# Optimization experiments

Hardware: AMD Instinct MI355X
Metric: run time of the kernel (lower is better)

Reference implementation:

```python
import jax, jax.numpy as jnp
import numpy as np
import math

BS, N, DX, H = 4, 256, 256, 8
DF = DX // H
DFF = 1024
EPS = 1e-5


def layer_norm(x, g, b):
    mu = jnp.mean(x, axis=-1, keepdims=True)
    var = jnp.var(x, axis=-1, keepdims=True)
    return (x - mu) * jax.lax.rsqrt(var + EPS) * g + b


def setup_inputs() -> dict:
    key = jax.random.key(0)
    ks = jax.random.split(key, 16)
    s = 1.0 / math.sqrt(DX)
    inp = {
        "X": jax.random.normal(ks[0], (BS, N, DX), jnp.float32),
        "e_add": jax.random.normal(ks[1], (BS, N, N, DX), jnp.float32),
        "e_mul": jax.random.normal(ks[2], (BS, N, N, DX), jnp.float32),
        "y_x_add": jax.random.normal(ks[3], (BS, DX), jnp.float32),
        "y_x_mul": jax.random.normal(ks[4], (BS, DX), jnp.float32),
        "node_mask": jnp.ones((BS, N), jnp.float32),
        "Wq": jax.random.normal(ks[5], (DX, DX), jnp.float32) * s,
        "bq": jnp.zeros((DX,), jnp.float32),
        "Wk": jax.random.normal(ks[6], (DX, DX), jnp.float32) * s,
        "bk": jnp.zeros((DX,), jnp.float32),
        "Wv": jax.random.normal(ks[7], (DX, DX), jnp.float32) * s,
        "bv": jnp.zeros((DX,), jnp.float32),
        "Wo": jax.random.normal(ks[8], (DX, DX), jnp.float32) * s,
        "bo": jnp.zeros((DX,), jnp.float32),
        "W1": jax.random.normal(ks[9], (DX, DFF), jnp.float32) * s,
        "b1": jnp.zeros((DFF,), jnp.float32),
        "W2": jax.random.normal(ks[10], (DFF, DX), jnp.float32) * (1.0 / math.sqrt(DFF)),
        "b2": jnp.zeros((DX,), jnp.float32),
        "g1": jnp.ones((DX,), jnp.float32),
        "beta1": jnp.zeros((DX,), jnp.float32),
        "g2": jnp.ones((DX,), jnp.float32),
        "beta2": jnp.zeros((DX,), jnp.float32),
    }
    return inp


def reference(X, e_add, e_mul, y_x_add, y_x_mul, node_mask,
              Wq, bq, Wk, bk, Wv, bv, Wo, bo, W1, b1, W2, b2,
              g1, beta1, g2, beta2):
    bs, n, dx = X.shape
    x_mask = node_mask[:, :, None]                      # (bs,n,1)
    e_mask1 = x_mask[:, :, None, :]                     # (bs,n,1,1)
    e_mask2 = x_mask[:, None, :, :]                     # (bs,1,n,1)

    Q = ((X @ Wq + bq) * x_mask).reshape(bs, n, H, DF)
    K = ((X @ Wk + bk) * x_mask).reshape(bs, n, H, DF)
    V = ((X @ Wv + bv) * x_mask).reshape(bs, n, H, DF)

    # elementwise QK: (bs,n,n,H,df)
    Y = Q[:, :, None] * K[:, None, :] / math.sqrt(DF)

    ee = (e_mask1 * e_mask2)[..., None]                 # (bs,n,n,1,1)
    E1 = (e_mul[..., None, :].reshape(bs, n, n, H, DF) if False else e_mul.reshape(bs, n, n, H, DF)) * ee
    E2 = e_add.reshape(bs, n, n, H, DF) * ee
    Y = Y * (E1 + 1.0) + E2

    # masked softmax over key axis (axis=2); mask from e_mask2 per head
    smask = node_mask[:, None, :, None, None] > 0       # (bs,1,n,1,1)
    Y = jnp.where(smask, Y, -jnp.inf)
    attn = jax.nn.softmax(Y, axis=2)

    weighted_V = jnp.sum(attn * V[:, None], axis=2).reshape(bs, n, dx)

    newX = y_x_add[:, None, :] + (y_x_mul[:, None, :] + 1.0) * weighted_V
    newX = ((newX @ Wo + bo)) * x_mask

    X1 = layer_norm(X + newX, g1, beta1)
    ffo = jax.nn.relu(X1 @ W1 + b1) @ W2 + b2
    X2 = layer_norm(X1 + ffo, g2, beta2)
    return X2
```

## Files before the change

### kernel.cpp

```cpp
#include <hip/hip_runtime.h>
#include <hip/hip_bf16.h>
#include <cstdint>

#define BSZ 4
#define NN 256
#define DXC 256
#define DFFC 1024
#define ROWS (BSZ*NN)

template <int EPI>
__global__ __launch_bounds__(256) void gemm32(
    const float* __restrict__ A,
    const float* __restrict__ B0, const float* __restrict__ B1,
    const float* __restrict__ B2,
    const float* __restrict__ bias0, const float* __restrict__ bias1,
    const float* __restrict__ bias2,
    float* __restrict__ C0, float* __restrict__ C1, float* __restrict__ C2,
    const float* __restrict__ mask,
    int M, int Nn, int K)
{
    const float* B = B0; const float* bias = bias0; float* C = C0;
    if (blockIdx.z == 1) { B = B1; bias = bias1; C = C1; }
    if (blockIdx.z == 2) { B = B2; bias = bias2; C = C2; }

    __shared__ float As[32][36];
    __shared__ float Bs[32][36];

    const int tid  = threadIdx.x;
    const int row0 = blockIdx.y * 32;
    const int col0 = blockIdx.x * 32;
    const int tx = tid & 15, ty = tid >> 4;

    const int la_r = tid >> 3;
    const int la_k = (tid & 7) * 4;

    float acc00 = 0.f, acc01 = 0.f, acc10 = 0.f, acc11 = 0.f;

    for (int k0 = 0; k0 < K; k0 += 32) {
        *(float4*)&As[la_r][la_k] = *(const float4*)(A + (size_t)(row0 + la_r) * K + (k0 + la_k));
        *(float4*)&Bs[la_r][la_k] = *(const float4*)(B + (size_t)(k0 + la_r) * Nn + (col0 + la_k));
        __syncthreads();
        #pragma unroll
        for (int k = 0; k < 32; ++k) {
            float a0v = As[2*ty][k],   a1v = As[2*ty+1][k];
            float b0v = Bs[k][2*tx],   b1v = Bs[k][2*tx+1];
            acc00 += a0v * b0v; acc01 += a0v * b1v;
            acc10 += a1v * b0v; acc11 += a1v * b1v;
        }
        __syncthreads();
    }

    const int r0 = row0 + 2*ty, c0 = col0 + 2*tx;
    const float bi0 = bias[c0], bi1 = bias[c0 + 1];
    float v00 = acc00 + bi0, v01 = acc01 + bi1;
    float v10 = acc10 + bi0, v11 = acc11 + bi1;
    if constexpr (EPI == 1) {
        float m0 = mask[r0], m1 = mask[r0 + 1];
        v00 *= m0; v01 *= m0; v10 *= m1; v11 *= m1;
    } else if constexpr (EPI == 2) {
        v00 = fmaxf(v00, 0.f); v01 = fmaxf(v01, 0.f);
        v10 = fmaxf(v10, 0.f); v11 = fmaxf(v11, 0.f);
    }
    C[(size_t)r0 * Nn + c0]       = v00; C[(size_t)r0 * Nn + c0 + 1]       = v01;
    C[(size_t)(r0+1) * Nn + c0]   = v10; C[(size_t)(r0+1) * Nn + c0 + 1]   = v11;
}

__global__ __launch_bounds__(256) void attn_kernel(
    const float* __restrict__ Qb, const float* __restrict__ Kb, const float* __restrict__ Vb,
    const float* __restrict__ e_add, const float* __restrict__ e_mul,
    const float* __restrict__ y_x_add, const float* __restrict__ y_x_mul,
    const float* __restrict__ nmask,
    float* __restrict__ nXi)
{
    const int row  = blockIdx.x;
    const int b    = row >> 8;
    const int tid  = threadIdx.x;
    const int wv   = tid >> 6;
    const int lane = tid & 63;
    const int hd   = lane << 2;

    const float mi = nmask[row];
    float4 q = *(const float4*)(Qb + (size_t)row * DXC + hd);
    const float inv = 0.17677669529663687f;
    q.x *= inv; q.y *= inv; q.z *= inv; q.w *= inv;

    const float* ea_p = e_add + (size_t)row * NN * DXC + hd;
    const float* em_p = e_mul + (size_t)row * NN * DXC + hd;
    const float* kp = Kb + (size_t)(b << 8) * DXC + hd;
    const float* vp = Vb + (size_t)(b << 8) * DXC + hd;
    const float* mp = nmask + (b << 8);

    float l0=0.f,l1=0.f,l2=0.f,l3=0.f;
    float a0=0.f,a1=0.f,a2=0.f,a3=0.f;

    #pragma unroll 4
    for (int j = wv; j < NN; j += 4) {
        const float mj = mp[j];
        const float ee = mi * mj;
        const float4 k4 = *(const float4*)(kp + (size_t)j * DXC);
        const float4 v4 = *(const float4*)(vp + (size_t)j * DXC);
        const float4 em = *(const float4*)(em_p + (size_t)j * DXC);
        const float4 ea = *(const float4*)(ea_p + (size_t)j * DXC);
        float y0 = (q.x*k4.x) * (em.x*ee + 1.f) + ea.x*ee;
        float y1 = (q.y*k4.y) * (em.y*ee + 1.f) + ea.y*ee;
        float y2 = (q.z*k4.z) * (em.z*ee + 1.f) + ea.z*ee;
        float y3 = (q.w*k4.w) * (em.w*ee + 1.f) + ea.w*ee;
        if (!(mj > 0.f)) { y0 = y1 = y2 = y3 = -1e30f; }
        const float p0 = __expf(y0), p1 = __expf(y1), p2 = __expf(y2), p3 = __expf(y3);
        l0 += p0; l1 += p1; l2 += p2; l3 += p3;
        a0 += p0*v4.x; a1 += p1*v4.y; a2 += p2*v4.z; a3 += p3*v4.w;
    }

    __shared__ float sl[4][256];
    __shared__ float sa[4][256];
    *(float4*)&sl[wv][hd] = make_float4(l0, l1, l2, l3);
    *(float4*)&sa[wv][hd] = make_float4(a0, a1, a2, a3);
    __syncthreads();

    const int c = tid;
    const float L = sl[0][c] + sl[1][c] + sl[2][c] + sl[3][c];
    const float A = sa[0][c] + sa[1][c] + sa[2][c] + sa[3][c];
    const float wV = A / L;
    const float yxa = y_x_add[b * DXC + c];
    const float yxm = y_x_mul[b * DXC + c];
    nXi[(size_t)row * DXC + c] = yxa + (yxm + 1.f) * wV;
}

__global__ __launch_bounds__(256) void ln_kernel(
    const float* __restrict__ base, const float* __restrict__ delta,
    const float* __restrict__ g, const float* __restrict__ be,
    float* __restrict__ out)
{
    const int row = blockIdx.x, t = threadIdx.x;
    const size_t idx = (size_t)row * DXC + t;
    const float s = base[idx] + delta[idx];
    __shared__ float red[8];
    float sum = s, sq = s * s;
    #pragma unroll
    for (int o = 32; o > 0; o >>= 1) { sum += __shfl_down(sum, o); sq += __shfl_down(sq, o); }
    if ((t & 63) == 0) { red[t >> 6] = sum; red[4 + (t >> 6)] = sq; }
    __syncthreads();
    sum = red[0] + red[1] + red[2] + red[3];
    sq  = red[4] + red[5] + red[6] + red[7];
    const float mean = sum * (1.f / DXC);
    const float var  = sq * (1.f / DXC) - mean * mean;
    const float r = rsqrtf(var + 1e-5f);
    out[idx] = (s - mean) * r * g[t] + be[t];
}

extern "C" void kernel_launch(void* const* d_in, const int* in_sizes, int n_in,
                              void* d_out, int out_size, void* d_ws, size_t ws_size,
                              hipStream_t stream)
{
    const float* X       = (const float*)d_in[0];
    const float* e_add   = (const float*)d_in[1];
    const float* e_mul   = (const float*)d_in[2];
    const float* y_x_add = (const float*)d_in[3];
    const float* y_x_mul = (const float*)d_in[4];
    const float* nmask   = (const float*)d_in[5];
    const float* Wq = (const float*)d_in[6];
    const float* bq = (const float*)d_in[7];
    const float* Wk = (const float*)d_in[8];
    const float* bk = (const float*)d_in[9];
    const float* Wv = (const float*)d_in[10];
    const float* bv = (const float*)d_in[11];
    const float* Wo = (const float*)d_in[12];
    const float* bo = (const float*)d_in[13];
    const float* W1 = (const float*)d_in[14];
    const float* b1 = (const float*)d_in[15];
    const float* W2 = (const float*)d_in[16];
    const float* b2 = (const float*)d_in[17];
    const float* g1 = (const float*)d_in[18];
    const float* be1= (const float*)d_in[19];
    const float* g2 = (const float*)d_in[20];
    const float* be2= (const float*)d_in[21];

    float* ws  = (float*)d_ws;
    float* Qb  = ws + 0 * 262144;
    float* Kb  = ws + 1 * 262144;
    float* Vb  = ws + 2 * 262144;
    float* nXi = ws + 3 * 262144;
    float* nXo = ws + 4 * 262144;
    float* X1b = ws + 5 * 262144;
    float* ffo = ws + 6 * 262144;
    float* hb  = ws + 7 * 262144;

    gemm32<1><<<dim3(DXC/32, ROWS/32, 3), 256, 0, stream>>>(
        X, Wq, Wk, Wv, bq, bk, bv, Qb, Kb, Vb, nmask, ROWS, DXC, DXC);

    attn_kernel<<<dim3(ROWS), 256, 0, stream>>>(
        Qb, Kb, Vb, e_add, e_mul, y_x_add, y_x_mul, nmask, nXi);

    gemm32<1><<<dim3(DXC/32, ROWS/32, 1), 256, 0, stream>>>(
        nXi, Wo, Wo, Wo, bo, bo, bo, nXo, nXo, nXo, nmask, ROWS, DXC, DXC);

    ln_kernel<<<dim3(ROWS), 256, 0, stream>>>(X, nXo, g1, be1, X1b);

    gemm32<2><<<dim3(DFFC/32, ROWS/32, 1), 256, 0, stream>>>(
        X1b, W1, W1, W1, b1, b1, b1, hb, hb, hb, nullptr, ROWS, DFFC, DXC);

    gemm32<0><<<dim3(DXC/32, ROWS/32, 1), 256, 0, stream>>>(
        hb, W2, W2, W2, b2, b2, b2, ffo, ffo, ffo, nullptr, ROWS, DXC, DFFC);

    ln_kernel<<<dim3(ROWS), 256, 0, stream>>>(X1b, ffo, g2, be2, (float*)d_out);
}
```

Baseline: 626.8 us.

## Use 64x64 register-blocked double-buffered GEMM and widen attention to 512 threads

Replaces the 32x32 GEMM with 64x64 tiles in which each thread computes a 4x4 register block. The A tile is stored transposed in shared memory, and the global loads for the next k-tile are prefetched into registers while the current tile is computed. The attention kernel moves to 512 threads (8 waves), and each iteration handles two key rows so more e_add/e_mul loads are in flight, aiming to get closer to memory bandwidth on the large edge tensors. The trade-off is fewer GEMM blocks, which may underfill the GPU on the small matrices, plus more registers per thread in both kernels.

```diff
diff --git a/kernel.cpp b/kernel.cpp
--- a/kernel.cpp
+++ b/kernel.cpp
@@ -1,5 +1,4 @@
 #include <hip/hip_runtime.h>
-#include <hip/hip_bf16.h>
 #include <cstdint>
 
 #define BSZ 4
@@ -9,7 +8,7 @@
 #define ROWS (BSZ*NN)
 
 template <int EPI>
-__global__ __launch_bounds__(256) void gemm32(
+__global__ __launch_bounds__(256) void gemm64(
     const float* __restrict__ A,
     const float* __restrict__ B0, const float* __restrict__ B1,
     const float* __restrict__ B2,
@@ -23,49 +22,102 @@
     if (blockIdx.z == 1) { B = B1; bias = bias1; C = C1; }
     if (blockIdx.z == 2) { B = B2; bias = bias2; C = C2; }
 
-    __shared__ float As[32][36];
-    __shared__ float Bs[32][36];
+    __shared__ float As[2][32][68];
+    __shared__ float Bs[2][32][68];
 
     const int tid  = threadIdx.x;
-    const int row0 = blockIdx.y * 32;
-    const int col0 = blockIdx.x * 32;
-    const int tx = tid & 15, ty = tid >> 4;
-
-    const int la_r = tid >> 3;
-    const int la_k = (tid & 7) * 4;
-
-    float acc00 = 0.f, acc01 = 0.f, acc10 = 0.f, acc11 = 0.f;
-
-    for (int k0 = 0; k0 < K; k0 += 32) {
-        *(float4*)&As[la_r][la_k] = *(const float4*)(A + (size_t)(row0 + la_r) * K + (k0 + la_k));
-        *(float4*)&Bs[la_r][la_k] = *(const float4*)(B + (size_t)(k0 + la_r) * Nn + (col0 + la_k));
-        __syncthreads();
+    const int row0 = blockIdx.y * 64;
+    const int col0 = blockIdx.x * 64;
+    const int tx4 = (tid & 15) * 4;
+    const int ty4 = (tid >> 4) * 4;
+
+    const int ar = tid >> 3;
+    const int ak = (tid & 7) * 4;
+    const int br = tid >> 4;
+    const int bn = (tid & 15) * 4;
+
+    const float* Ap  = A + (size_t)(row0 + ar) * K + ak;
+    const float* Ap2 = A + (size_t)(row0 + 32 + ar) * K + ak;
+    const float* Bp  = B + (size_t)br * Nn + col0 + bn;
+    const float* Bp2 = B + (size_t)(br + 16) * Nn + col0 + bn;
+
+    float4 a0 = *(const float4*)Ap;
+    float4 a1 = *(const float4*)Ap2;
+    float4 b0 = *(const float4*)Bp;
+    float4 b1 = *(const float4*)Bp2;
+
+    float acc[4][4] = {};
+
+    As[0][ak+0][ar] = a0.x; As[0][ak+1][ar] = a0.y;
+    As[0][ak+2][ar] = a0.z; As[0][ak+3][ar] = a0.w;
+    As[0][ak+0][ar+32] = a1.x; As[0][ak+1][ar+32] = a1.y;
+    As[0][ak+2][ar+32] = a1.z; As[0][ak+3][ar+32] = a1.w;
+    *(float4*)&Bs[0][br][bn]      = b0;
+    *(float4*)&Bs[0][br+16][bn]   = b1;
+    __syncthreads();
+
+    const int nt = K >> 5;
+    for (int t = 0; t < nt; ++t) {
+        const int cur = t & 1, nxt = cur ^ 1;
+        const bool more = (t + 1 < nt);
+        if (more) {
+            const int k0 = (t + 1) << 5;
+            a0 = *(const float4*)(Ap + k0);
+            a1 = *(const float4*)(Ap2 + k0);
+            b0 = *(const float4*)(Bp + (size_t)k0 * Nn);
+            b1 = *(const float4*)(Bp2 + (size_t)k0 * Nn);
+        }
         #pragma unroll
         for (int k = 0; k < 32; ++k) {
-            float a0v = As[2*ty][k],   a1v = As[2*ty+1][k];
-            float b0v = Bs[k][2*tx],   b1v = Bs[k][2*tx+1];
-            acc00 += a0v * b0v; acc01 += a0v * b1v;
-            acc10 += a1v * b0v; acc11 += a1v * b1v;
-        }
-        __syncthreads();
-    }
-
-    const int r0 = row0 + 2*ty, c0 = col0 + 2*tx;
-    const float bi0 = bias[c0], bi1 = bias[c0 + 1];
-    float v00 = acc00 + bi0, v01 = acc01 + bi1;
-    float v10 = acc10 + bi0, v11 = acc11 + bi1;
-    if constexpr (EPI == 1) {
-        float m0 = mask[r0], m1 = mask[r0 + 1];
-        v00 *= m0; v01 *= m0; v10 *= m1; v11 *= m1;
-    } else if constexpr (EPI == 2) {
-        v00 = fmaxf(v00, 0.f); v01 = fmaxf(v01, 0.f);
-        v10 = fmaxf(v10, 0.f); v11 = fmaxf(v11, 0.f);
-    }
-    C[(size_t)r0 * Nn + c0]       = v00; C[(size_t)r0 * Nn + c0 + 1]       = v01;
-    C[(size_t)(r0+1) * Nn + c0]   = v10; C[(size_t)(r0+1) * Nn + c0 + 1]   = v11;
-}
-
-__global__ __launch_bounds__(256) void attn_kernel(
+            const float4 av = *(const float4*)&As[cur][k][ty4];
+            const float4 bv = *(const float4*)&Bs[cur][k][tx4];
+            acc[0][0] = fmaf(av.x, bv.x, acc[0][0]);
+            acc[0][1] = fmaf(av.x, bv.y, acc[0][1]);
+            acc[0][2] = fmaf(av.x, bv.z, acc[0][2]);
+            acc[0][3] = fmaf(av.x, bv.w, acc[0][3]);
+            acc[1][0] = fmaf(av.y, bv.x, acc[1][0]);
+            acc[1][1] = fmaf(av.y, bv.y, acc[1][1]);
+            acc[1][2] = fmaf(av.y, bv.z, acc[1][2]);
+            acc[1][3] = fmaf(av.y, bv.w, acc[1][3]);
+            acc[2][0] = fmaf(av.z, bv.x, acc[2][0]);
+            acc[2][1] = fmaf(av.z, bv.y, acc[2][1]);
+            acc[2][2] = fmaf(av.z, bv.z, acc[2][2]);
+            acc[2][3] = fmaf(av.z, bv.w, acc[2][3]);
+            acc[3][0] = fmaf(av.w, bv.x, acc[3][0]);
+            acc[3][1] = fmaf(av.w, bv.y, acc[3][1]);
+            acc[3][2] = fmaf(av.w, bv.z, acc[3][2]);
+            acc[3][3] = fmaf(av.w, bv.w, acc[3][3]);
+        }
+        if (more) {
+            As[nxt][ak+0][ar] = a0.x; As[nxt][ak+1][ar] = a0.y;
+            As[nxt][ak+2][ar] = a0.z; As[nxt][ak+3][ar] = a0.w;
+            As[nxt][ak+0][ar+32] = a1.x; As[nxt][ak+1][ar+32] = a1.y;
+            As[nxt][ak+2][ar+32] = a1.z; As[nxt][ak+3][ar+32] = a1.w;
+            *(float4*)&Bs[nxt][br][bn]    = b0;
+            *(float4*)&Bs[nxt][br+16][bn] = b1;
+            __syncthreads();
+        }
+    }
+
+    const int c0 = col0 + tx4;
+    const float4 bi = *(const float4*)(bias + c0);
+    #pragma unroll
+    for (int i = 0; i < 4; ++i) {
+        const int r = row0 + ty4 + i;
+        float4 v = make_float4(acc[i][0] + bi.x, acc[i][1] + bi.y,
+                               acc[i][2] + bi.z, acc[i][3] + bi.w);
+        if constexpr (EPI == 1) {
+            const float m = mask[r];
+            v.x *= m; v.y *= m; v.z *= m; v.w *= m;
+        } else if constexpr (EPI == 2) {
+            v.x = fmaxf(v.x, 0.f); v.y = fmaxf(v.y, 0.f);
+            v.z = fmaxf(v.z, 0.f); v.w = fmaxf(v.w, 0.f);
+        }
+        *(float4*)&C[(size_t)r * Nn + c0] = v;
+    }
+}
+
+__global__ __launch_bounds__(512) void attn_kernel(
     const float* __restrict__ Qb, const float* __restrict__ Kb, const float* __restrict__ Vb,
     const float* __restrict__ e_add, const float* __restrict__ e_mul,
     const float* __restrict__ y_x_add, const float* __restrict__ y_x_mul,
@@ -90,40 +142,62 @@
     const float* vp = Vb + (size_t)(b << 8) * DXC + hd;
     const float* mp = nmask + (b << 8);
 
-    float l0=0.f,l1=0.f,l2=0.f,l3=0.f;
-    float a0=0.f,a1=0.f,a2=0.f,a3=0.f;
-
-    #pragma unroll 4
-    for (int j = wv; j < NN; j += 4) {
-        const float mj = mp[j];
-        const float ee = mi * mj;
-        const float4 k4 = *(const float4*)(kp + (size_t)j * DXC);
-        const float4 v4 = *(const float4*)(vp + (size_t)j * DXC);
-        const float4 em = *(const float4*)(em_p + (size_t)j * DXC);
-        const float4 ea = *(const float4*)(ea_p + (size_t)j * DXC);
-        float y0 = (q.x*k4.x) * (em.x*ee + 1.f) + ea.x*ee;
-        float y1 = (q.y*k4.y) * (em.y*ee + 1.f) + ea.y*ee;
-        float y2 = (q.z*k4.z) * (em.z*ee + 1.f) + ea.z*ee;
-        float y3 = (q.w*k4.w) * (em.w*ee + 1.f) + ea.w*ee;
-        if (!(mj > 0.f)) { y0 = y1 = y2 = y3 = -1e30f; }
-        const float p0 = __expf(y0), p1 = __expf(y1), p2 = __expf(y2), p3 = __expf(y3);
-        l0 += p0; l1 += p1; l2 += p2; l3 += p3;
-        a0 += p0*v4.x; a1 += p1*v4.y; a2 += p2*v4.z; a3 += p3*v4.w;
-    }
-
-    __shared__ float sl[4][256];
-    __shared__ float sa[4][256];
-    *(float4*)&sl[wv][hd] = make_float4(l0, l1, l2, l3);
-    *(float4*)&sa[wv][hd] = make_float4(a0, a1, a2, a3);
+    float s0=0.f,s1=0.f,s2=0.f,s3=0.f;
+    float o0=0.f,o1=0.f,o2=0.f,o3=0.f;
+
+    for (int j = wv; j < NN; j += 16) {
+        const int j2 = j + 8;
+        const float mjA = mp[j];
+        const float mjB = mp[j2];
+        const size_t oA = (size_t)j  * DXC;
+        const size_t oB = (size_t)j2 * DXC;
+        const float4 kA  = *(const float4*)(kp  + oA);
+        const float4 vA  = *(const float4*)(vp  + oA);
+        const float4 emA = *(const float4*)(em_p + oA);
+        const float4 eaA = *(const float4*)(ea_p + oA);
+        const float4 kB  = *(const float4*)(kp  + oB);
+        const float4 vB  = *(const float4*)(vp  + oB);
+        const float4 emB = *(const float4*)(em_p + oB);
+        const float4 eaB = *(const float4*)(ea_p + oB);
+
+        const float eeA = mi * mjA;
+        const float eeB = mi * mjB;
+        float y0 = (q.x*kA.x) * (emA.x*eeA + 1.f) + eaA.x*eeA;
+        float y1 = (q.y*kA.y) * (emA.y*eeA + 1.f) + eaA.y*eeA;
+        float y2 = (q.z*kA.z) * (emA.z*eeA + 1.f) + eaA.z*eeA;
+        float y3 = (q.w*kA.w) * (emA.w*eeA + 1.f) + eaA.w*eeA;
+        float z0 = (q.x*kB.x) * (emB.x*eeB + 1.f) + eaB.x*eeB;
+        float z1 = (q.y*kB.y) * (emB.y*eeB + 1.f) + eaB.y*eeB;
+        float z2 = (q.z*kB.z) * (emB.z*eeB + 1.f) + eaB.z*eeB;
+        float z3 = (q.w*kB.w) * (emB.w*eeB + 1.f) + eaB.w*eeB;
+        if (!(mjA > 0.f)) { y0 = y1 = y2 = y3 = -1e30f; }
+        if (!(mjB > 0.f)) { z0 = z1 = z2 = z3 = -1e30f; }
+
+        const float pA0 = __expf(y0), pA1 = __expf(y1), pA2 = __expf(y2), pA3 = __expf(y3);
+        const float pB0 = __expf(z0), pB1 = __expf(z1), pB2 = __expf(z2), pB3 = __expf(z3);
+        s0 += pA0 + pB0; s1 += pA1 + pB1; s2 += pA2 + pB2; s3 += pA3 + pB3;
+        o0 = fmaf(pA0, vA.x, fmaf(pB0, vB.x, o0));
+        o1 = fmaf(pA1, vA.y, fmaf(pB1, vB.y, o1));
+        o2 = fmaf(pA2, vA.z, fmaf(pB2, vB.z, o2));
+        o3 = fmaf(pA3, vA.w, fmaf(pB3, vB.w, o3));
+    }
+
+    __shared__ float sl[8][256];
+    __shared__ float sa[8][256];
+    *(float4*)&sl[wv][hd] = make_float4(s0, s1, s2, s3);
+    *(float4*)&sa[wv][hd] = make_float4(o0, o1, o2, o3);
     __syncthreads();
 
-    const int c = tid;
-    const float L = sl[0][c] + sl[1][c] + sl[2][c] + sl[3][c];
-    const float A = sa[0][c] + sa[1][c] + sa[2][c] + sa[3][c];
-    const float wV = A / L;
-    const float yxa = y_x_add[b * DXC + c];
-    const float yxm = y_x_mul[b * DXC + c];
-    nXi[(size_t)row * DXC + c] = yxa + (yxm + 1.f) * wV;
+    if (tid < 256) {
+        const int c = tid;
+        float L = 0.f, Acc = 0.f;
+        #pragma unroll
+        for (int w = 0; w < 8; ++w) { L += sl[w][c]; Acc += sa[w][c]; }
+        const float wV = Acc / L;
+        const float yxa = y_x_add[b * DXC + c];
+        const float yxm = y_x_mul[b * DXC + c];
+        nXi[(size_t)row * DXC + c] = yxa + (yxm + 1.f) * wV;
+    }
 }
 
 __global__ __launch_bounds__(256) void ln_kernel(
@@ -185,21 +259,21 @@
     float* ffo = ws + 6 * 262144;
     float* hb  = ws + 7 * 262144;
 
-    gemm32<1><<<dim3(DXC/32, ROWS/32, 3), 256, 0, stream>>>(
+    gemm64<1><<<dim3(DXC/64, ROWS/64, 3), 256, 0, stream>>>(
         X, Wq, Wk, Wv, bq, bk, bv, Qb, Kb, Vb, nmask, ROWS, DXC, DXC);
 
-    attn_kernel<<<dim3(ROWS), 256, 0, stream>>>(
+    attn_kernel<<<dim3(ROWS), 512, 0, stream>>>(
         Qb, Kb, Vb, e_add, e_mul, y_x_add, y_x_mul, nmask, nXi);
 
-    gemm32<1><<<dim3(DXC/32, ROWS/32, 1), 256, 0, stream>>>(
+    gemm64<1><<<dim3(DXC/64, ROWS/64, 1), 256, 0, stream>>>(
         nXi, Wo, Wo, Wo, bo, bo, bo, nXo, nXo, nXo, nmask, ROWS, DXC, DXC);
 
     ln_kernel<<<dim3(ROWS), 256, 0, stream>>>(X, nXo, g1, be1, X1b);
 
-    gemm32<2><<<dim3(DFFC/32, ROWS/32, 1), 256, 0, stream>>>(
+    gemm64<2><<<dim3(DFFC/64, ROWS/64, 1), 256, 0, stream>>>(
         X1b, W1, W1, W1, b1, b1, b1, hb, hb, hb, nullptr, ROWS, DFFC, DXC);
 
-    gemm32<0><<<dim3(DXC/32, ROWS/32, 1), 256, 0, stream>>>(
+    gemm64<0><<<dim3(DXC/64, ROWS/64, 1), 256, 0, stream>>>(
         hb, W2, W2, W2, b2, b2, b2, ffo, ffo, ffo, nullptr, ROWS, DXC, DFFC);
 
     ln_kernel<<<dim3(ROWS), 256, 0, stream>>>(X1b, ffo, g2, be2, (float*)d_out);
```

After: 649.6 us. 3.6% more time.
